# Optimization experiments

Hardware: AMD Instinct MI355X
Metric: run time of the kernel (lower is better)

Reference implementation:

```python
import jax, jax.numpy as jnp
import numpy as np

N_HEADS = 16
D_HEAD = 64
TOKENS_PER_FRAME = 128
ROPE_THETA = 10000.0


def setup_inputs() -> dict:
    key = jax.random.key(0)
    ks = jax.random.split(key, 4)
    B, L, D = 2, 2048, 1024
    x = jax.random.normal(ks[0], (B, L, D), dtype=jnp.float32)
    W_qkv = jax.random.normal(ks[1], (3 * D, D), dtype=jnp.float32) * (1.0 / np.sqrt(D))
    b_qkv = jnp.zeros((3 * D,), dtype=jnp.float32)
    W_out = jax.random.normal(ks[2], (D, D), dtype=jnp.float32) * (1.0 / np.sqrt(D))
    b_out = jnp.zeros((D,), dtype=jnp.float32)
    q_gamma = jnp.ones((D_HEAD,), dtype=jnp.float32)
    k_gamma = jnp.ones((D_HEAD,), dtype=jnp.float32)
    return {"x": x, "W_qkv": W_qkv, "b_qkv": b_qkv, "W_out": W_out,
            "b_out": b_out, "q_gamma": q_gamma, "k_gamma": k_gamma}


def _rms_norm(t, gamma, eps=1e-6):
    # RMSNorm over the head dim (QKNorm)
    var = jnp.mean(jnp.square(t), axis=-1, keepdims=True)
    return t * jax.lax.rsqrt(var + eps) * gamma


def _rope(t, pos):
    # t: [B,H,L,dh], pos: [L] absolute positions (with kv-cache offset applied)
    dh = t.shape[-1]
    half = dh // 2
    inv_freq = 1.0 / (ROPE_THETA ** (jnp.arange(half, dtype=jnp.float32) / half))
    angles = pos[:, None].astype(jnp.float32) * inv_freq[None, :]  # [L, half]
    cos = jnp.cos(angles)[None, None]  # [1,1,L,half]
    sin = jnp.sin(angles)[None, None]
    t1, t2 = t[..., :half], t[..., half:]
    return jnp.concatenate([t1 * cos - t2 * sin, t2 * cos + t1 * sin], axis=-1)


def _block_causal_mask(L, tokens_per_frame, n_cached=0):
    total = n_cached + L
    n_frames = total // tokens_per_frame
    fq = (jnp.arange(L) + n_cached) // tokens_per_frame          # [L] query frames
    fk = jnp.arange(total) // tokens_per_frame                    # [total] key frames
    allow = fk[None, :] <= fq[:, None]
    allow &= ~((fq[:, None] == n_frames - 1) & (fk[None, :] == 0))
    return allow  # [L, total] bool


def reference(x, W_qkv, b_qkv, W_out, b_out, q_gamma, k_gamma):
    B, L, D = x.shape
    H, dh = N_HEADS, D_HEAD
    qkv = x @ W_qkv.T + b_qkv                                    # [B,L,3D]
    qkv = qkv.reshape(B, L, 3, H, dh).transpose(2, 0, 3, 1, 4)   # [3,B,H,L,dh]
    q, k, v = qkv[0], qkv[1], qkv[2]
    q = _rms_norm(q, q_gamma)
    k = _rms_norm(k, k_gamma)
    offset = 0  # no kv_cache (prefill)
    pos = jnp.arange(L) + offset
    q = _rope(q, pos)
    k = _rope(k, jnp.arange(offset + L))
    scale = 1.0 / np.sqrt(dh)
    scores = jnp.einsum('bhqd,bhkd->bhqk', q, k) * scale
    mask = _block_causal_mask(L, TOKENS_PER_FRAME, offset)        # [L, L+offset]
    scores = jnp.where(mask[None, None], scores, jnp.finfo(scores.dtype).min)
    probs = jax.nn.softmax(scores, axis=-1)
    attn = jnp.einsum('bhqk,bhkd->bhqd', probs, v)                # [B,H,L,dh]
    attn = attn.transpose(0, 2, 1, 3).reshape(B, L, D)
    return attn @ W_out.T + b_out
```

## Files before the change

### kernel.cpp

```cpp
#include <hip/hip_runtime.h>
#include <hip/hip_bf16.h>

typedef __bf16 bf16x8 __attribute__((ext_vector_type(8)));
typedef __bf16 bf16x4 __attribute__((ext_vector_type(4)));
typedef float  f32x4  __attribute__((ext_vector_type(4)));

#define GLOBAL_AS __attribute__((address_space(1)))
#define LDS_AS    __attribute__((address_space(3)))

__device__ __forceinline__ void glds16(const void* g, void* l) {
  __builtin_amdgcn_global_load_lds((const GLOBAL_AS void*)g, (LDS_AS void*)l, 16, 0, 0);
}

__global__ __launch_bounds__(256) void prep_kernel(
    const float* __restrict__ a, __bf16* __restrict__ da, int na4,
    const float* __restrict__ b, __bf16* __restrict__ db, int nb4,
    const float* __restrict__ c, __bf16* __restrict__ dc, int nc4,
    float2* __restrict__ tab) {
  int i = blockIdx.x * 256 + threadIdx.x;
  const float* s; __bf16* d; int j = i;
  if (i < na4) { s = a; d = da; }
  else if ((j = i - na4) < nb4) { s = b; d = db; }
  else if ((j = i - na4 - nb4) < nc4) { s = c; d = dc; }
  else {
    j = i - na4 - nb4 - nc4;
    if (j < 65536) {
      int l = j >> 5, jj = j & 31;
      float inv = 1.0f / powf(10000.0f, (float)jj * (1.0f / 32.0f));
      float ang = (float)l * inv;
      tab[j] = make_float2(cosf(ang), sinf(ang));
    }
    return;
  }
  float4 f = ((const float4*)s)[j];
  bf16x4 o;
  o[0] = (__bf16)f.x; o[1] = (__bf16)f.y; o[2] = (__bf16)f.z; o[3] = (__bf16)f.w;
  ((bf16x4*)d)[j] = o;
}

template <int EPI, int TM>
__global__ __launch_bounds__(512) void gemm_bt(
    const __bf16* __restrict__ A, const __bf16* __restrict__ Bm, int K, int nbn,
    const float* __restrict__ bias,
    __bf16* __restrict__ qo, __bf16* __restrict__ ko, __bf16* __restrict__ vo,
    float* __restrict__ out,
    const float* __restrict__ qg, const float* __restrict__ kg,
    const float2* __restrict__ tab) {
  constexpr int WR = TM / 32;
  constexpr int WC = 8 / WR;
  constexpr int NPW = 128 / WC;
  constexpr int NI = NPW / 16;
  constexpr int ACH = TM * 8;
  __shared__ __bf16 As[TM * 64];
  __shared__ __bf16 Bs[128 * 64];
  const int t = threadIdx.x;
  const int nwg = gridDim.x;
  const int id = blockIdx.x;
  const int swz = (id & 7) * (nwg >> 3) + (id >> 3);
  const int bn = swz % nbn, bm = swz / nbn;
  const int lane = t & 63, w = t >> 6;
  const int wr = w / WC, wc = w % WC;
  const int lr = lane & 15, lg = lane >> 4;
  const size_t rowA0 = (size_t)bm * TM, rowB0 = (size_t)bn * 128;

  f32x4 acc[2][NI] = {};

  for (int k0 = 0; k0 < K; k0 += 64) {
    __syncthreads();
#pragma unroll
    for (int c0 = 0; c0 < ACH + 1024; c0 += 512) {
      int c = c0 + t;
      if (c0 < ACH) {
        int row = c >> 3, sl = c & 7, sp = sl ^ (row & 7);
        glds16(A + (rowA0 + row) * K + k0 + sp * 8, As + c * 8);
      } else {
        int c2 = c - ACH;
        int row = c2 >> 3, sl = c2 & 7, sp = sl ^ (row & 7);
        glds16(Bm + (rowB0 + row) * K + k0 + sp * 8, Bs + c2 * 8);
      }
    }
    __syncthreads();
#pragma unroll
    for (int kk = 0; kk < 2; ++kk) {
      bf16x8 af[2], bfr[NI];
#pragma unroll
      for (int i = 0; i < 2; ++i) {
        int ar = wr * 32 + i * 16 + lr;
        af[i] = *(const bf16x8*)&As[ar * 64 + (((kk * 4 + lg) ^ (ar & 7)) * 8)];
      }
#pragma unroll
      for (int i = 0; i < NI; ++i) {
        int br = wc * NPW + i * 16 + lr;
        bfr[i] = *(const bf16x8*)&Bs[br * 64 + (((kk * 4 + lg) ^ (br & 7)) * 8)];
      }
#pragma unroll
      for (int mi = 0; mi < 2; ++mi)
#pragma unroll
        for (int ni = 0; ni < NI; ++ni)
          acc[mi][ni] = __builtin_amdgcn_mfma_f32_16x16x32_bf16(af[mi], bfr[ni], acc[mi][ni], 0, 0, 0);
    }
  }

  if constexpr (EPI == 0) {
    const int sect = bn >> 3;
    const int h = (bn * 2 + wc) & 15;
    float bbv[NI];
#pragma unroll
    for (int ni = 0; ni < NI; ++ni) bbv[ni] = bias[bn * 128 + wc * NPW + ni * 16 + lr];
    if (sect < 2) {
      __bf16* dst = sect ? ko : qo;
      const float* g = sect ? kg : qg;
      float gam[NI];
#pragma unroll
      for (int ni = 0; ni < NI; ++ni) gam[ni] = g[ni * 16 + lr];
      float ss[2][4];
#pragma unroll
      for (int mi = 0; mi < 2; ++mi)
#pragma unroll
        for (int r = 0; r < 4; ++r) {
          float s = 0.0f;
#pragma unroll
          for (int ni = 0; ni < NI; ++ni) {
            acc[mi][ni][r] += bbv[ni];
            s += acc[mi][ni][r] * acc[mi][ni][r];
          }
          ss[mi][r] = s;
        }
#pragma unroll
      for (int step = 1; step <= 8; step <<= 1)
#pragma unroll
        for (int mi = 0; mi < 2; ++mi)
#pragma unroll
          for (int r = 0; r < 4; ++r)
            ss[mi][r] += __shfl_xor(ss[mi][r], step);
#pragma unroll
      for (int mi = 0; mi < 2; ++mi) {
#pragma unroll
        for (int r = 0; r < 4; ++r) {
          int m = bm * TM + wr * 32 + mi * 16 + lg * 4 + r;
          int b_ = m >> 11, l = m & 2047;
          float rinv = rsqrtf(ss[mi][r] * (1.0f / 64.0f) + 1e-6f);
          float v0 = acc[mi][0][r] * rinv * gam[0];
          float v1 = acc[mi][1][r] * rinv * gam[1];
          float v2 = acc[mi][2][r] * rinv * gam[2];
          float v3 = acc[mi][3][r] * rinv * gam[3];
          float2 cs0 = tab[l * 32 + lr];
          float2 cs1 = tab[l * 32 + 16 + lr];
          float o0 = v0 * cs0.x - v2 * cs0.y;
          float o2 = v2 * cs0.x + v0 * cs0.y;
          float o1 = v1 * cs1.x - v3 * cs1.y;
          float o3 = v3 * cs1.x + v1 * cs1.y;
          size_t base = ((size_t)(b_ * 16 + h) * 2048 + l) * 64;
          dst[base + lr]      = (__bf16)o0;
          dst[base + 16 + lr] = (__bf16)o1;
          dst[base + 32 + lr] = (__bf16)o2;
          dst[base + 48 + lr] = (__bf16)o3;
        }
      }
    } else {
#pragma unroll
      for (int mi = 0; mi < 2; ++mi) {
#pragma unroll
        for (int ni = 0; ni < NI; ++ni) {
          int d = ni * 16 + lr;
#pragma unroll
          for (int r = 0; r < 4; ++r) {
            int m = bm * TM + wr * 32 + mi * 16 + lg * 4 + r;
            int b_ = m >> 11, l = m & 2047;
            vo[((size_t)((b_ * 16 + h) * 64 + d)) * 2048 + l] = (__bf16)(acc[mi][ni][r] + bbv[ni]);
          }
        }
      }
    }
  } else {
#pragma unroll
    for (int mi = 0; mi < 2; ++mi) {
      int m0 = bm * TM + wr * 32 + mi * 16 + lg * 4;
#pragma unroll
      for (int ni = 0; ni < NI; ++ni) {
        int n = bn * 128 + wc * NPW + ni * 16 + lr;
        float bb = bias[n];
#pragma unroll
        for (int r = 0; r < 4; ++r)
          out[(size_t)(m0 + r) * 1024 + n] = acc[mi][ni][r] + bb;
      }
    }
  }
}

__global__ __launch_bounds__(512, 4) void attn_kernel(
    const __bf16* __restrict__ qb, const __bf16* __restrict__ kb,
    const __bf16* __restrict__ vT, __bf16* __restrict__ ob) {
  __shared__ char smem[65536];
  char* Kl = smem;
  char* Vl = smem + 16384;

  const int id = blockIdx.x;
  const int rank = (id < 256) ? id : 767 - id;
  const int fq = rank >> 5;
  const int bh = rank & 31;
  const int t = threadIdx.x;
  const int lane = t & 63;
  const int w = t >> 6;
  const int qq = w & 3;
  const int half = w >> 2;
  const int lr = lane & 15, lg = lane >> 4;
  const size_t hoff = (size_t)bh * (2048 * 64);
  const int q0 = fq * 128 + qq * 32;
  char* Pw = smem + 32768 + w * 4096;

  const int fkS = (fq == 15) ? 2 : 0;
  const int niter = (fq + 1) - (fq == 15 ? 1 : 0);

  bf16x8 aq[2][2];
#pragma unroll
  for (int kk = 0; kk < 2; ++kk)
#pragma unroll
    for (int mf = 0; mf < 2; ++mf)
      aq[kk][mf] = *(const bf16x8*)(qb + hoff + (size_t)(q0 + mf * 16 + lr) * 64 + kk * 32 + lg * 8);

  {
    int c = t, row = c >> 3, sl = c & 7, sp = sl ^ (row & 7);
    glds16(kb + hoff + (size_t)((fkS) * 64 + row) * 64 + sp * 8,         Kl + c * 16);
    glds16(kb + hoff + (size_t)((fkS + niter) * 64 + row) * 64 + sp * 8, Kl + 8192 + c * 16);
    glds16(vT + hoff + (size_t)row * 2048 + (fkS) * 64 + sp * 8,         Vl + c * 16);
    glds16(vT + hoff + (size_t)row * 2048 + (fkS + niter) * 64 + sp * 8, Vl + 8192 + c * 16);
  }
  __syncthreads();

  f32x4 acc[2][4] = {};
  float m_run[2] = {-INFINITY, -INFINITY};
  float l_run[2] = {0.0f, 0.0f};

  for (int it = 0; it < niter; ++it) {
    const bool pref = (it + 1 < niter);
    bf16x8 rK0, rK1, rV0, rV1;
    if (pref) {
      int c = t, row = c >> 3, sl = c & 7, sp = sl ^ (row & 7);
      rK0 = *(const bf16x8*)(kb + hoff + (size_t)((fkS + it + 1) * 64 + row) * 64 + sp * 8);
      rK1 = *(const bf16x8*)(kb + hoff + (size_t)((fkS + niter + it + 1) * 64 + row) * 64 + sp * 8);
      rV0 = *(const bf16x8*)(vT + hoff + (size_t)row * 2048 + (fkS + it + 1) * 64 + sp * 8);
      rV1 = *(const bf16x8*)(vT + hoff + (size_t)row * 2048 + (fkS + niter + it + 1) * 64 + sp * 8);
    }
    char* Kc = Kl + half * 8192;
    char* Vc = Vl + half * 8192;

    f32x4 st[2][4] = {};
    __builtin_amdgcn_s_setprio(1);
#pragma unroll
    for (int kk = 0; kk < 2; ++kk)
#pragma unroll
      for (int nf = 0; nf < 4; ++nf) {
        int rk = nf * 16 + lr;
        bf16x8 bk = *(const bf16x8*)(Kc + rk * 128 + (((kk * 4 + lg) ^ (rk & 7)) << 4));
        st[0][nf] = __builtin_amdgcn_mfma_f32_16x16x32_bf16(bk, aq[kk][0], st[0][nf], 0, 0, 0);
        st[1][nf] = __builtin_amdgcn_mfma_f32_16x16x32_bf16(bk, aq[kk][1], st[1][nf], 0, 0, 0);
      }
    __builtin_amdgcn_s_setprio(0);

#pragma unroll
    for (int mf = 0; mf < 2; ++mf) {
      float mx = st[mf][0][0];
#pragma unroll
      for (int nf = 0; nf < 4; ++nf)
#pragma unroll
        for (int r = 0; r < 4; ++r) mx = fmaxf(mx, st[mf][nf][r]);
      mx *= 0.125f;
      mx = fmaxf(mx, __shfl_xor(mx, 16));
      mx = fmaxf(mx, __shfl_xor(mx, 32));
      float mnew = m_run[mf], cr = 1.0f;
      if (__any(mx > m_run[mf] + 8.0f)) {
        mnew = fmaxf(m_run[mf], mx);
        cr = __expf(m_run[mf] - mnew);
#pragma unroll
        for (int df = 0; df < 4; ++df) acc[mf][df] *= cr;
      }
      float lsum = 0.0f;
#pragma unroll
      for (int nf = 0; nf < 4; ++nf)
#pragma unroll
        for (int r = 0; r < 4; ++r) {
          float p = __expf(fmaf(st[mf][nf][r], 0.125f, -mnew));
          st[mf][nf][r] = p;
          lsum += p;
        }
      lsum += __shfl_xor(lsum, 16);
      lsum += __shfl_xor(lsum, 32);
      l_run[mf] = l_run[mf] * cr + lsum;
      m_run[mf] = mnew;

#pragma unroll
      for (int nf = 0; nf < 4; ++nf) {
        int row = mf * 16 + lr;
        bf16x4 pw;
#pragma unroll
        for (int r = 0; r < 4; ++r) pw[r] = (__bf16)st[mf][nf][r];
        int slot = nf * 2 + (lg >> 1);
        *(bf16x4*)(Pw + row * 128 + (((slot ^ (lr & 7)) << 4) | ((lg & 1) * 8))) = pw;
      }
    }

    __builtin_amdgcn_s_setprio(1);
#pragma unroll
    for (int kk = 0; kk < 2; ++kk) {
      bf16x8 ap[2];
#pragma unroll
      for (int mf = 0; mf < 2; ++mf) {
        int row = mf * 16 + lr;
        ap[mf] = *(const bf16x8*)(Pw + row * 128 + (((kk * 4 + lg) ^ (lr & 7)) << 4));
      }
#pragma unroll
      for (int df = 0; df < 4; ++df) {
        int rv = df * 16 + lr;
        bf16x8 av = *(const bf16x8*)(Vc + rv * 128 + (((kk * 4 + lg) ^ (rv & 7)) << 4));
        acc[0][df] = __builtin_amdgcn_mfma_f32_16x16x32_bf16(av, ap[0], acc[0][df], 0, 0, 0);
        acc[1][df] = __builtin_amdgcn_mfma_f32_16x16x32_bf16(av, ap[1], acc[1][df], 0, 0, 0);
      }
    }
    __builtin_amdgcn_s_setprio(0);

    __syncthreads();
    if (pref) {
      int c = t;
      *(bf16x8*)(Kl + c * 16)        = rK0;
      *(bf16x8*)(Kl + 8192 + c * 16) = rK1;
      *(bf16x8*)(Vl + c * 16)        = rV0;
      *(bf16x8*)(Vl + 8192 + c * 16) = rV1;
      __syncthreads();
    }
  }

  __syncthreads();
  if (half == 1) {
    char* Ob = smem + qq * 8192;
#pragma unroll
    for (int mf = 0; mf < 2; ++mf)
#pragma unroll
      for (int df = 0; df < 4; ++df)
        *(f32x4*)(Ob + (mf * 4 + df) * 1024 + lane * 16) = acc[mf][df];
    if (lg == 0) {
#pragma unroll
      for (int mf = 0; mf < 2; ++mf)
        *(float2*)(smem + 32768 + qq * 1024 + mf * 128 + lr * 8) =
            make_float2(m_run[mf], l_run[mf]);
    }
  }
  __syncthreads();
  if (half == 0) {
    char* Ob = smem + qq * 8192;
    const int b = bh >> 4, h = bh & 15;
#pragma unroll
    for (int mf = 0; mf < 2; ++mf) {
      float2 ml1 = *(const float2*)(smem + 32768 + qq * 1024 + mf * 128 + lr * 8);
      float m = fmaxf(m_run[mf], ml1.x);
      float a0 = __expf(m_run[mf] - m);
      float a1 = __expf(ml1.x - m);
      float linv = 1.0f / (l_run[mf] * a0 + ml1.y * a1);
      int l = q0 + mf * 16 + lr;
#pragma unroll
      for (int df = 0; df < 4; ++df) {
        f32x4 o1 = *(const f32x4*)(Ob + (mf * 4 + df) * 1024 + lane * 16);
        bf16x4 ov;
#pragma unroll
        for (int r = 0; r < 4; ++r)
          ov[r] = (__bf16)((acc[mf][df][r] * a0 + o1[r] * a1) * linv);
        int d0 = df * 16 + lg * 4;
        *(bf16x4*)(ob + ((size_t)(b * 2048 + l)) * 1024 + h * 64 + d0) = ov;
      }
    }
  }
}

extern "C" void kernel_launch(void* const* d_in, const int* in_sizes, int n_in,
                              void* d_out, int out_size, void* d_ws, size_t ws_size,
                              hipStream_t stream) {
  (void)in_sizes; (void)n_in; (void)out_size; (void)ws_size;
  const float* x    = (const float*)d_in[0];
  const float* Wqkv = (const float*)d_in[1];
  const float* bqkv = (const float*)d_in[2];
  const float* Wout = (const float*)d_in[3];
  const float* bout = (const float*)d_in[4];
  const float* qg   = (const float*)d_in[5];
  const float* kg   = (const float*)d_in[6];

  char* ws = (char*)d_ws;
  __bf16* xb   = (__bf16*)(ws);
  __bf16* wqb  = (__bf16*)(ws + 8388608);
  __bf16* wob  = (__bf16*)(ws + 14680064);
  __bf16* qbuf = (__bf16*)(ws + 16777216);
  __bf16* kbuf = (__bf16*)(ws + 25165824);
  __bf16* vbuf = (__bf16*)(ws + 33554432);
  __bf16* aob  = (__bf16*)(ws + 41943040);
  float2* rtab = (float2*)(ws + 50331648);

  prep_kernel<<<8448, 256, 0, stream>>>(x, xb, 1048576, Wqkv, wqb, 786432,
                                        Wout, wob, 262144, rtab);
  gemm_bt<0, 128><<<768, 512, 0, stream>>>(xb, wqb, 1024, 24, bqkv, qbuf, kbuf, vbuf, nullptr,
                                           qg, kg, rtab);
  attn_kernel<<<512, 512, 0, stream>>>(qbuf, kbuf, vbuf, aob);
  gemm_bt<1, 64><<<512, 512, 0, stream>>>(aob, wob, 1024, 8, bout, nullptr, nullptr, nullptr,
                                          (float*)d_out, nullptr, nullptr, nullptr);
}
```

Baseline: 192.6 us.

## Triple-buffer GEMM K-loop with async LDS loads and vmcnt waits

Restructures the bf16 GEMM main loop into a three-stage ring of LDS buffers with K-step 32. Loads for step i+2 are issued while the MFMAs for step i run, so global-to-LDS traffic overlaps compute. The two __syncthreads per step become one barrier gated by s_waitcnt vmcnt counts. The XOR swizzle is redone for 32-wide rows. In exchange there are twice as many loop iterations, and correctness depends on hand-tuned waitcnt values that differ by warp when TM is 64.

```diff
diff --git a/kernel.cpp b/kernel.cpp
--- a/kernel.cpp
+++ b/kernel.cpp
@@ -50,9 +50,10 @@
   constexpr int WC = 8 / WR;
   constexpr int NPW = 128 / WC;
   constexpr int NI = NPW / 16;
-  constexpr int ACH = TM * 8;
-  __shared__ __bf16 As[TM * 64];
-  __shared__ __bf16 Bs[128 * 64];
+  constexpr int ACH = TM * 4;
+  constexpr int BCH = 512;
+  __shared__ __bf16 As[3][TM * 32];
+  __shared__ __bf16 Bs[3][128 * 32];
   const int t = threadIdx.x;
   const int nwg = gridDim.x;
   const int id = blockIdx.x;
@@ -63,42 +64,61 @@
   const int lr = lane & 15, lg = lane >> 4;
   const size_t rowA0 = (size_t)bm * TM, rowB0 = (size_t)bn * 128;
 
+  auto STAGE = [&](int buf, int k0) {
+#pragma unroll
+    for (int c0 = 0; c0 < ACH + BCH; c0 += 512) {
+      int c = c0 + t;
+      if (c < ACH) {
+        int row = c >> 2, q = c & 3, sl = q ^ ((row >> 1) & 3);
+        glds16(A + (rowA0 + row) * K + k0 + sl * 8, &As[buf][c * 8]);
+      } else if (c < ACH + BCH) {
+        int c2 = c - ACH;
+        int row = c2 >> 2, q = c2 & 3, sl = q ^ ((row >> 1) & 3);
+        glds16(Bm + (rowB0 + row) * K + k0 + sl * 8, &Bs[buf][c2 * 8]);
+      }
+    }
+  };
+
   f32x4 acc[2][NI] = {};
 
-  for (int k0 = 0; k0 < K; k0 += 64) {
-    __syncthreads();
-#pragma unroll
-    for (int c0 = 0; c0 < ACH + 1024; c0 += 512) {
-      int c = c0 + t;
-      if (c0 < ACH) {
-        int row = c >> 3, sl = c & 7, sp = sl ^ (row & 7);
-        glds16(A + (rowA0 + row) * K + k0 + sp * 8, As + c * 8);
-      } else {
-        int c2 = c - ACH;
-        int row = c2 >> 3, sl = c2 & 7, sp = sl ^ (row & 7);
-        glds16(Bm + (rowB0 + row) * K + k0 + sp * 8, Bs + c2 * 8);
-      }
-    }
-    __syncthreads();
-#pragma unroll
-    for (int kk = 0; kk < 2; ++kk) {
-      bf16x8 af[2], bfr[NI];
-#pragma unroll
-      for (int i = 0; i < 2; ++i) {
-        int ar = wr * 32 + i * 16 + lr;
-        af[i] = *(const bf16x8*)&As[ar * 64 + (((kk * 4 + lg) ^ (ar & 7)) * 8)];
-      }
-#pragma unroll
-      for (int i = 0; i < NI; ++i) {
-        int br = wc * NPW + i * 16 + lr;
-        bfr[i] = *(const bf16x8*)&Bs[br * 64 + (((kk * 4 + lg) ^ (br & 7)) * 8)];
-      }
-#pragma unroll
-      for (int mi = 0; mi < 2; ++mi)
-#pragma unroll
-        for (int ni = 0; ni < NI; ++ni)
-          acc[mi][ni] = __builtin_amdgcn_mfma_f32_16x16x32_bf16(af[mi], bfr[ni], acc[mi][ni], 0, 0, 0);
-    }
+  STAGE(0, 0);
+  STAGE(1, 32);
+  const int niter = K >> 5;
+  int cur = 0;
+  for (int i = 0; i < niter; ++i) {
+    if (i + 1 < niter) {
+      if (TM == 64 && w >= 4) asm volatile("s_waitcnt vmcnt(1)" ::: "memory");
+      else                    asm volatile("s_waitcnt vmcnt(2)" ::: "memory");
+    } else {
+      asm volatile("s_waitcnt vmcnt(0)" ::: "memory");
+    }
+    __builtin_amdgcn_s_barrier();
+    asm volatile("" ::: "memory");
+
+    bf16x8 af[2], bfr[NI];
+#pragma unroll
+    for (int mi = 0; mi < 2; ++mi) {
+      int ar = wr * 32 + mi * 16 + lr;
+      af[mi] = *(const bf16x8*)&As[cur][ar * 32 + ((lg ^ ((ar >> 1) & 3)) * 8)];
+    }
+#pragma unroll
+    for (int ni = 0; ni < NI; ++ni) {
+      int br = wc * NPW + ni * 16 + lr;
+      bfr[ni] = *(const bf16x8*)&Bs[cur][br * 32 + ((lg ^ ((br >> 1) & 3)) * 8)];
+    }
+
+    if (i + 2 < niter) {
+      int nxt = cur + 2; if (nxt >= 3) nxt -= 3;
+      STAGE(nxt, (i + 2) << 5);
+    }
+
+#pragma unroll
+    for (int mi = 0; mi < 2; ++mi)
+#pragma unroll
+      for (int ni = 0; ni < NI; ++ni)
+        acc[mi][ni] = __builtin_amdgcn_mfma_f32_16x16x32_bf16(af[mi], bfr[ni], acc[mi][ni], 0, 0, 0);
+
+    ++cur; if (cur == 3) cur = 0;
   }
 
   if constexpr (EPI == 0) {
```

Result: faster. 187.5 us (-2.6%).
